# Kernel optimization log

Measured on AMD Instinct MI355X. Metric: run time of the kernel, lower is better.

## Reference

```python
import math
import jax, jax.numpy as jnp
import numpy as np

N_HEAD = 16
N_GROUPS = 32
EPS = 1e-05


def gelu(x):
    return 0.5 * x * (1.0 + jnp.tanh(math.sqrt(2.0 / math.pi) * (x + 0.044715 * x ** 3)))


def dp_group_norm(x, weight, bias, num_groups=N_GROUPS, eps=EPS):
    # x: [B, T, H]. torch F.group_norm on transposed [B, H, T] normalizes over
    # (channels_per_group, T) jointly per (batch, group).
    B, T, H = x.shape
    xg = x.reshape(B, T, num_groups, H // num_groups)
    mean = jnp.mean(xg, axis=(1, 3), keepdims=True)
    var = jnp.mean((xg - mean) ** 2, axis=(1, 3), keepdims=True)
    xn = ((xg - mean) / jnp.sqrt(var + eps)).reshape(B, T, H)
    return xn * weight + bias


def attention(x, w_attn, b_attn, w_aproj, b_aproj):
    B, T, H = x.shape
    hd = H // N_HEAD
    qkv = x @ w_attn + b_attn                      # [B, T, 3H]
    q, k, v = jnp.split(qkv, 3, axis=-1)
    q = q.reshape(B, T, N_HEAD, hd).transpose(0, 2, 1, 3)   # [B, nh, T, hd]
    k = k.reshape(B, T, N_HEAD, hd).transpose(0, 2, 1, 3)   # [B, nh, T, hd]
    v = v.reshape(B, T, N_HEAD, hd).transpose(0, 2, 1, 3)
    w = jnp.einsum('bhqd,bhkd->bhqk', q, k)        # no 1/sqrt(d): scale=False
    causal = jnp.tril(jnp.ones((T, T), dtype=x.dtype))
    w = w * causal - 1e10 * (1.0 - causal)
    w = jax.nn.softmax(w, axis=-1)
    a = jnp.einsum('bhqk,bhkd->bhqd', w, v)        # [B, nh, T, hd]
    a = a.transpose(0, 2, 1, 3).reshape(B, T, H)
    a = a @ w_aproj + b_aproj
    present = jnp.stack((k, v))                    # [2, B, nh, T, hd]
    return a, present


def setup_inputs() -> dict:
    key = jax.random.key(0)
    ks = jax.random.split(key, 6)
    B, T, H = 2, 2048, 1024
    return {
        'x': jax.random.normal(ks[0], (B, T, H), dtype=jnp.float32),
        'w_attn': jax.random.normal(ks[1], (H, 3 * H), dtype=jnp.float32) * 0.02,
        'b_attn': jnp.zeros((3 * H,), dtype=jnp.float32),
        'w_aproj': jax.random.normal(ks[2], (H, H), dtype=jnp.float32) * 0.02,
        'b_aproj': jnp.zeros((H,), dtype=jnp.float32),
        'ln1_w': jnp.ones((H,), dtype=jnp.float32),
        'ln1_b': jnp.zeros((H,), dtype=jnp.float32),
        'ln2_w': jnp.ones((H,), dtype=jnp.float32),
        'ln2_b': jnp.zeros((H,), dtype=jnp.float32),
        'w_fc': jax.random.normal(ks[3], (H, 4 * H), dtype=jnp.float32) * 0.02,
        'b_fc': jnp.zeros((4 * H,), dtype=jnp.float32),
        'w_mproj': jax.random.normal(ks[4], (4 * H, H), dtype=jnp.float32) * 0.02,
        'b_mproj': jnp.zeros((H,), dtype=jnp.float32),
    }


def reference(x, w_attn, b_attn, w_aproj, b_aproj, ln1_w, ln1_b, ln2_w, ln2_b,
              w_fc, b_fc, w_mproj, b_mproj):
    a, present = attention(dp_group_norm(x, ln1_w, ln1_b), w_attn, b_attn, w_aproj, b_aproj)
    x = x + a
    h = gelu(dp_group_norm(x, ln2_w, ln2_b) @ w_fc + b_fc)
    m = h @ w_mproj + b_mproj
    x = x + m
    return (x, present)
```

## Files before the change

kernel.cpp:

```cpp
#include <hip/hip_runtime.h>

#define B_  2
#define T_  2048
#define H_  1024
#define NH_ 16
#define HD_ 64
#define M_  (B_*T_)
#define PS_ 72

typedef __bf16 bf16x8 __attribute__((ext_vector_type(8)));
typedef float  floatx4 __attribute__((ext_vector_type(4)));

typedef __attribute__((address_space(1))) const unsigned int gas_u32;
typedef __attribute__((address_space(3))) unsigned int       las_u32;

__device__ __forceinline__ void gload_lds16(const __bf16* g, __bf16* l) {
    __builtin_amdgcn_global_load_lds((gas_u32*)g, (las_u32*)l, 16, 0, 0);
}

__global__ __launch_bounds__(256) void transpose_bf16(
    const float* __restrict__ in, __bf16* __restrict__ out, int K, int N)
{
    __shared__ float tile[32][33];
    const int k0 = blockIdx.x * 32, n0 = blockIdx.y * 32;
    const int tx = threadIdx.x & 31, ty = threadIdx.x >> 5;
#pragma unroll
    for (int i = 0; i < 32; i += 8)
        tile[ty + i][tx] = in[(size_t)(k0 + ty + i) * N + (n0 + tx)];
    __syncthreads();
#pragma unroll
    for (int i = 0; i < 32; i += 8)
        out[(size_t)(n0 + ty + i) * K + (k0 + tx)] = (__bf16)tile[tx][ty + i];
}

__global__ __launch_bounds__(256) void gn_partial(
    const float* __restrict__ x, float2* __restrict__ part)
{
    const int bg = blockIdx.x, chunk = blockIdx.y;
    const int batch = bg >> 5, g = bg & 31;
    const float* xp = x + (size_t)batch * T_ * H_ + g * 32;
    float s = 0.f, ss = 0.f;
    for (int i = threadIdx.x; i < 128 * 32; i += 256) {
        const int t = chunk * 128 + (i >> 5), c = i & 31;
        const float v = xp[(size_t)t * H_ + c];
        s += v; ss += v * v;
    }
#pragma unroll
    for (int off = 32; off > 0; off >>= 1) {
        s  += __shfl_down(s,  off, 64);
        ss += __shfl_down(ss, off, 64);
    }
    __shared__ float rs[4], rss[4];
    const int wv = threadIdx.x >> 6, lane = threadIdx.x & 63;
    if (lane == 0) { rs[wv] = s; rss[wv] = ss; }
    __syncthreads();
    if (threadIdx.x == 0)
        part[bg * 16 + chunk] =
            make_float2(rs[0] + rs[1] + rs[2] + rs[3],
                        rss[0] + rss[1] + rss[2] + rss[3]);
}

__global__ __launch_bounds__(64) void gn_finalize(
    const float2* __restrict__ part, float2* __restrict__ stats)
{
    const int bg = threadIdx.x;
    float s = 0.f, ss = 0.f;
#pragma unroll
    for (int i = 0; i < 16; ++i) {
        const float2 p = part[bg * 16 + i];
        s += p.x; ss += p.y;
    }
    const float inv = 1.f / (float)(T_ * 32);
    const float mean = s * inv;
    const float var  = ss * inv - mean * mean;
    stats[bg] = make_float2(mean, rsqrtf(var + 1e-5f));
}

__global__ __launch_bounds__(256) void gn_apply(
    const float* __restrict__ x, const float2* __restrict__ stats,
    const float* __restrict__ w, const float* __restrict__ bsc,
    __bf16* __restrict__ out)
{
    const size_t idx = ((size_t)blockIdx.x * 256 + threadIdx.x) * 4;
    const int h = (int)(idx & (H_ - 1));
    const int batch = (int)(idx >> 21);
    const float2 mr = stats[batch * 32 + (h >> 5)];
    const float4 xv = *(const float4*)(x + idx);
    const float4 wv = *(const float4*)(w + h);
    const float4 bv = *(const float4*)(bsc + h);
    __bf16 o[4];
    o[0] = (__bf16)((xv.x - mr.x) * mr.y * wv.x + bv.x);
    o[1] = (__bf16)((xv.y - mr.x) * mr.y * wv.y + bv.y);
    o[2] = (__bf16)((xv.z - mr.x) * mr.y * wv.z + bv.z);
    o[3] = (__bf16)((xv.w - mr.x) * mr.y * wv.w + bv.w);
    *(uint2*)(out + idx) = *(uint2*)o;
}

__device__ __forceinline__ void gemm_core(
    const __bf16* __restrict__ A, const __bf16* __restrict__ BT,
    int K, int m0, int n0, __bf16* As, __bf16* Bs, floatx4 (&acc)[4][4])
{
    const int tid  = threadIdx.x;
    const int lane = tid & 63, wv = tid >> 6;
    const int quad = lane >> 4, l16 = lane & 15;
    const int wm = (wv >> 1) * 64, wn = (wv & 1) * 64;
    const int r0 = tid >> 2, c0 = (tid & 3) * 8;

    const __bf16* Ag = A  + (size_t)(m0 + r0) * K + c0;
    const __bf16* Bg = BT + (size_t)(n0 + r0) * K + c0;

    for (int kt = 0; kt < K; kt += 64) {
        __syncthreads();
#pragma unroll
        for (int s = 0; s < 2; ++s) {
            gload_lds16(Ag + kt + s * 32,                As + s * 4096 + tid * 8);
            gload_lds16(Ag + (size_t)64 * K + kt + s * 32, As + s * 4096 + 2048 + tid * 8);
            gload_lds16(Bg + kt + s * 32,                Bs + s * 4096 + tid * 8);
            gload_lds16(Bg + (size_t)64 * K + kt + s * 32, Bs + s * 4096 + 2048 + tid * 8);
        }
        __syncthreads();
#pragma unroll
        for (int kk = 0; kk < 2; ++kk) {
            bf16x8 af[4], bfg[4];
#pragma unroll
            for (int i = 0; i < 4; ++i)
                af[i]  = *(const bf16x8*)(As + kk * 4096 + (wm + i * 16 + l16) * 32 + quad * 8);
#pragma unroll
            for (int i = 0; i < 4; ++i)
                bfg[i] = *(const bf16x8*)(Bs + kk * 4096 + (wn + i * 16 + l16) * 32 + quad * 8);
#pragma unroll
            for (int mi = 0; mi < 4; ++mi)
#pragma unroll
                for (int ni = 0; ni < 4; ++ni)
                    acc[mi][ni] = __builtin_amdgcn_mfma_f32_16x16x32_bf16(
                        af[mi], bfg[ni], acc[mi][ni], 0, 0, 0);
        }
    }
}

#define GEMM_PROLOGUE(KVAL)                                             \
    __shared__ __align__(16) __bf16 As[2 * 4096], Bs[2 * 4096];         \
    const int m0 = blockIdx.x * 128, n0 = blockIdx.y * 128;             \
    floatx4 acc[4][4];                                                  \
    { floatx4 z = {0.f, 0.f, 0.f, 0.f};                                 \
      for (int i = 0; i < 4; ++i) for (int j = 0; j < 4; ++j) acc[i][j] = z; } \
    gemm_core(A, BT, (KVAL), m0, n0, As, Bs, acc);                      \
    const int tid = threadIdx.x, lane = tid & 63, wv = tid >> 6;        \
    const int quad = lane >> 4, l16 = lane & 15;                        \
    const int wm = (wv >> 1) * 64, wn = (wv & 1) * 64;                  \
    (void)tid;

__global__ __launch_bounds__(256) void gemm_qkv(
    const __bf16* __restrict__ A, const __bf16* __restrict__ BT,
    const float* __restrict__ bias, __bf16* __restrict__ qb,
    __bf16* __restrict__ kb, __bf16* __restrict__ vtb,
    float* __restrict__ present)
{
    GEMM_PROLOGUE(H_)
#pragma unroll
    for (int ni = 0; ni < 4; ++ni) {
        const int col = n0 + wn + ni * 16 + l16;
        const float bv = bias[col];
        const int which = col >> 10, c = col & 1023, hh = c >> 6, d = c & 63;
#pragma unroll
        for (int mi = 0; mi < 4; ++mi)
#pragma unroll
            for (int r = 0; r < 4; ++r) {
                const int row = m0 + wm + mi * 16 + quad * 4 + r;
                const int bb = row >> 11, t = row & 2047;
                const float v = acc[mi][ni][r] + bv;
                const size_t idx = (((size_t)bb * NH_ + hh) * T_ + t) * HD_ + d;
                if (which == 0)      qb[idx] = (__bf16)(v * 1.4426950408889634f);
                else if (which == 1) { kb[idx] = (__bf16)v; present[idx] = v; }
                else { vtb[(((size_t)bb * NH_ + hh) * HD_ + d) * T_ + t] = (__bf16)v;
                       present[(size_t)B_ * NH_ * T_ * HD_ + idx] = v; }
            }
    }
}

__global__ __launch_bounds__(256) void gemm_gelu(
    const __bf16* __restrict__ A, const __bf16* __restrict__ BT,
    const float* __restrict__ bias, __bf16* __restrict__ out)
{
    GEMM_PROLOGUE(H_)
#pragma unroll
    for (int ni = 0; ni < 4; ++ni) {
        const int col = n0 + wn + ni * 16 + l16;
        const float bv = bias[col];
#pragma unroll
        for (int mi = 0; mi < 4; ++mi)
#pragma unroll
            for (int r = 0; r < 4; ++r) {
                const int row = m0 + wm + mi * 16 + quad * 4 + r;
                const float v = acc[mi][ni][r] + bv;
                const float g = 0.5f * v *
                    (1.f + tanhf(0.7978845608028654f * (v + 0.044715f * v * v * v)));
                out[(size_t)row * (4 * H_) + col] = (__bf16)g;
            }
    }
}

__global__ __launch_bounds__(256) void gemm_resid_n64(
    const __bf16* __restrict__ A, const __bf16* __restrict__ BT,
    const float* __restrict__ bias, const float* __restrict__ resid,
    float* __restrict__ out, int K, int N)
{
    __shared__ __align__(16) __bf16 As[2 * 4096], Bs[2 * 2048];
    const int m0 = blockIdx.x * 128, n0 = blockIdx.y * 64;
    const int tid  = threadIdx.x;
    const int lane = tid & 63, wv = tid >> 6;
    const int quad = lane >> 4, l16 = lane & 15;
    const int wm = (wv >> 1) * 64, wn = (wv & 1) * 32;
    const int r0 = tid >> 2, c0 = (tid & 3) * 8;

    floatx4 acc[4][2];
    { floatx4 z = {0.f, 0.f, 0.f, 0.f};
#pragma unroll
      for (int i = 0; i < 4; ++i) { acc[i][0] = z; acc[i][1] = z; } }

    const __bf16* Ag = A  + (size_t)(m0 + r0) * K + c0;
    const __bf16* Bg = BT + (size_t)(n0 + r0) * K + c0;

    for (int kt = 0; kt < K; kt += 64) {
        __syncthreads();
#pragma unroll
        for (int s = 0; s < 2; ++s) {
            gload_lds16(Ag + kt + s * 32,                  As + s * 4096 + tid * 8);
            gload_lds16(Ag + (size_t)64 * K + kt + s * 32, As + s * 4096 + 2048 + tid * 8);
            gload_lds16(Bg + kt + s * 32,                  Bs + s * 2048 + tid * 8);
        }
        __syncthreads();
#pragma unroll
        for (int kk = 0; kk < 2; ++kk) {
            bf16x8 af[4], bfg[2];
#pragma unroll
            for (int i = 0; i < 4; ++i)
                af[i]  = *(const bf16x8*)(As + kk * 4096 + (wm + i * 16 + l16) * 32 + quad * 8);
#pragma unroll
            for (int i = 0; i < 2; ++i)
                bfg[i] = *(const bf16x8*)(Bs + kk * 2048 + (wn + i * 16 + l16) * 32 + quad * 8);
#pragma unroll
            for (int mi = 0; mi < 4; ++mi)
#pragma unroll
                for (int ni = 0; ni < 2; ++ni)
                    acc[mi][ni] = __builtin_amdgcn_mfma_f32_16x16x32_bf16(
                        af[mi], bfg[ni], acc[mi][ni], 0, 0, 0);
        }
    }

#pragma unroll
    for (int ni = 0; ni < 2; ++ni) {
        const int col = n0 + wn + ni * 16 + l16;
        const float bv = bias[col];
#pragma unroll
        for (int mi = 0; mi < 4; ++mi)
#pragma unroll
            for (int r = 0; r < 4; ++r) {
                const int row = m0 + wm + mi * 16 + quad * 4 + r;
                const size_t idx = (size_t)row * N + col;
                out[idx] = acc[mi][ni][r] + bv + resid[idx];
            }
    }
}

__global__ __launch_bounds__(256) void attn_kernel(
    const __bf16* __restrict__ qb, const __bf16* __restrict__ kb,
    const __bf16* __restrict__ vtb, __bf16* __restrict__ aout)
{
    const int bh = blockIdx.x;
    const int sp = 31 - blockIdx.y;
    const int bb = bh >> 4, hh = bh & 15;
    const __bf16* Q  = qb  + (size_t)bh * T_ * HD_;
    const __bf16* Kp = kb  + (size_t)bh * T_ * HD_;
    const __bf16* VT = vtb + (size_t)bh * HD_ * T_;
    __shared__ __align__(16) __bf16 Qs[2 * 2048];
    __shared__ __align__(16) __bf16 Ks[2][2 * 2048];
    __shared__ __align__(16) __bf16 Vs[2][2 * 2048];
    __shared__ __align__(16) __bf16 Ps[64 * PS_];

    const int tid = threadIdx.x, lane = tid & 63, wv = tid >> 6;
    const int quad = lane >> 4, l16 = lane & 15;
    const int sr = tid >> 2;
    const int scs = (((tid & 3) ^ ((sr >> 1) & 3)) * 8);
    const int xq8 = (quad ^ ((l16 >> 1) & 3)) * 8;

    const int q0 = sp * 64, nkt = sp + 1;

#pragma unroll
    for (int s = 0; s < 2; ++s) {
        gload_lds16(Q  + (size_t)(q0 + sr) * HD_ + s * 32 + scs, Qs + s * 2048 + tid * 8);
        gload_lds16(Kp + (size_t)sr * HD_ + s * 32 + scs, &Ks[0][s * 2048 + tid * 8]);
        gload_lds16(VT + (size_t)sr * T_  + s * 32 + scs, &Vs[0][s * 2048 + tid * 8]);
    }
    asm volatile("s_waitcnt vmcnt(0)" ::: "memory");
    __builtin_amdgcn_s_barrier();
    __builtin_amdgcn_sched_barrier(0);

    bf16x8 aq[2];
#pragma unroll
    for (int kk = 0; kk < 2; ++kk)
        aq[kk] = *(const bf16x8*)(Qs + kk * 2048 + (wv * 16 + l16) * 32 + xq8);

    float m_i[4], l_p[4];
    floatx4 Ov[4];
    { floatx4 z = {0.f, 0.f, 0.f, 0.f};
#pragma unroll
      for (int i = 0; i < 4; ++i) { Ov[i] = z; m_i[i] = -1e30f; l_p[i] = 0.f; } }

    int cur = 0;
    for (int kt = 0; kt < nkt; ++kt) {
        if (kt + 1 < nkt) {
            const int kn = (kt + 1) * 64;
#pragma unroll
            for (int s = 0; s < 2; ++s) {
                gload_lds16(Kp + (size_t)(kn + sr) * HD_ + s * 32 + scs,
                            &Ks[cur ^ 1][s * 2048 + tid * 8]);
                gload_lds16(VT + (size_t)sr * T_ + kn + s * 32 + scs,
                            &Vs[cur ^ 1][s * 2048 + tid * 8]);
            }
            asm volatile("s_waitcnt vmcnt(4)" ::: "memory");
        } else {
            asm volatile("s_waitcnt vmcnt(0)" ::: "memory");
        }
        __builtin_amdgcn_s_barrier();
        __builtin_amdgcn_sched_barrier(0);

        const __bf16* Kc = Ks[cur];
        const __bf16* Vc = Vs[cur];

        floatx4 sacc[4];
        { floatx4 z = {0.f, 0.f, 0.f, 0.f};
#pragma unroll
          for (int i = 0; i < 4; ++i) sacc[i] = z; }
#pragma unroll
        for (int kk = 0; kk < 2; ++kk)
#pragma unroll
            for (int ni = 0; ni < 4; ++ni) {
                const bf16x8 bk = *(const bf16x8*)(Kc + kk * 2048 + (ni * 16 + l16) * 32 + xq8);
                sacc[ni] = __builtin_amdgcn_mfma_f32_16x16x32_bf16(aq[kk], bk, sacc[ni], 0, 0, 0);
            }
        if (kt == sp) {
#pragma unroll
            for (int ni = 0; ni < 4; ++ni) {
                const int keyL = ni * 16 + l16;
#pragma unroll
                for (int r = 0; r < 4; ++r)
                    if (keyL > quad * 4 + r + wv * 16) sacc[ni][r] = -1e30f;
            }
        }
        float rmax[4];
#pragma unroll
        for (int r = 0; r < 4; ++r)
            rmax[r] = fmaxf(fmaxf(sacc[0][r], sacc[1][r]),
                            fmaxf(sacc[2][r], sacc[3][r]));
#pragma unroll
        for (int off = 1; off < 16; off <<= 1)
#pragma unroll
            for (int r = 0; r < 4; ++r)
                rmax[r] = fmaxf(rmax[r], __shfl_xor(rmax[r], off, 64));
        float need = rmax[0] - m_i[0];
#pragma unroll
        for (int r = 1; r < 4; ++r) need = fmaxf(need, rmax[r] - m_i[r]);
        if (__any(need > 8.f)) {
#pragma unroll
            for (int r = 0; r < 4; ++r) {
                const float mn = fmaxf(m_i[r], rmax[r]);
                const float al = exp2f(m_i[r] - mn);
                m_i[r] = mn;
                l_p[r] *= al;
#pragma unroll
                for (int ni = 0; ni < 4; ++ni) Ov[ni][r] *= al;
            }
        }
#pragma unroll
        for (int ni = 0; ni < 4; ++ni)
#pragma unroll
            for (int r = 0; r < 4; ++r) {
                const float pe = exp2f(sacc[ni][r] - m_i[r]);
                sacc[ni][r] = pe;
                l_p[r] += pe;
            }
#pragma unroll
        for (int ni = 0; ni < 4; ++ni)
#pragma unroll
            for (int r = 0; r < 4; ++r)
                Ps[(wv * 16 + quad * 4 + r) * PS_ + ni * 16 + l16] = (__bf16)sacc[ni][r];
#pragma unroll
        for (int kk = 0; kk < 2; ++kk) {
            const bf16x8 ap = *(const bf16x8*)(Ps + (wv * 16 + l16) * PS_ + kk * 32 + quad * 8);
#pragma unroll
            for (int ni = 0; ni < 4; ++ni) {
                const bf16x8 bv2 = *(const bf16x8*)(Vc + kk * 2048 + (ni * 16 + l16) * 32 + xq8);
                Ov[ni] = __builtin_amdgcn_mfma_f32_16x16x32_bf16(ap, bv2, Ov[ni], 0, 0, 0);
            }
        }
        __builtin_amdgcn_sched_barrier(0);
        __builtin_amdgcn_s_barrier();
        __builtin_amdgcn_sched_barrier(0);
        cur ^= 1;
    }
#pragma unroll
    for (int off = 1; off < 16; off <<= 1)
#pragma unroll
        for (int r = 0; r < 4; ++r)
            l_p[r] += __shfl_xor(l_p[r], off, 64);
#pragma unroll
    for (int ni = 0; ni < 4; ++ni)
#pragma unroll
        for (int r = 0; r < 4; ++r) {
            const int t = q0 + wv * 16 + quad * 4 + r;
            aout[((size_t)(bb * T_ + t)) * H_ + hh * HD_ + ni * 16 + l16] =
                (__bf16)(Ov[ni][r] / l_p[r]);
        }
}

extern "C" void kernel_launch(void* const* d_in, const int* in_sizes, int n_in,
                              void* d_out, int out_size, void* d_ws, size_t ws_size,
                              hipStream_t stream)
{
    (void)in_sizes; (void)n_in; (void)out_size; (void)ws_size;
    const float* x       = (const float*)d_in[0];
    const float* w_attn  = (const float*)d_in[1];
    const float* b_attn  = (const float*)d_in[2];
    const float* w_aproj = (const float*)d_in[3];
    const float* b_aproj = (const float*)d_in[4];
    const float* ln1_w   = (const float*)d_in[5];
    const float* ln1_b   = (const float*)d_in[6];
    const float* ln2_w   = (const float*)d_in[7];
    const float* ln2_b   = (const float*)d_in[8];
    const float* w_fc    = (const float*)d_in[9];
    const float* b_fc    = (const float*)d_in[10];
    const float* w_mproj = (const float*)d_in[11];
    const float* b_mproj = (const float*)d_in[12];
    float* out = (float*)d_out;
    float* present = out + (size_t)M_ * H_;

    char* wp = (char*)d_ws;
    auto alloc = [&](size_t bytes) {
        void* p = (void*)wp; wp += (bytes + 255) & ~(size_t)255; return p;
    };
    __bf16* A1       = (__bf16*)alloc((size_t)M_ * H_ * 2);
    __bf16* A2       = (__bf16*)alloc((size_t)M_ * H_ * 2);
    __bf16* WattnT   = (__bf16*)alloc((size_t)3 * H_ * H_ * 2);
    __bf16* WaprojT  = (__bf16*)alloc((size_t)H_ * H_ * 2);
    __bf16* WfcT     = (__bf16*)alloc((size_t)4 * H_ * H_ * 2);
    __bf16* WmprojT  = (__bf16*)alloc((size_t)4 * H_ * H_ * 2);
    __bf16* qb       = (__bf16*)alloc((size_t)M_ * H_ * 2);
    __bf16* kb       = (__bf16*)alloc((size_t)M_ * H_ * 2);
    __bf16* vtb      = (__bf16*)alloc((size_t)M_ * H_ * 2);
    __bf16* attn_out = (__bf16*)alloc((size_t)M_ * H_ * 2);
    float*  x2       = (float*) alloc((size_t)M_ * H_ * 4);
    __bf16* Hbuf     = (__bf16*)alloc((size_t)M_ * 4 * H_ * 2);
    float2* gn_part  = (float2*)alloc(64 * 16 * sizeof(float2));
    float2* gn_stats = (float2*)alloc(64 * sizeof(float2));

    transpose_bf16<<<dim3(H_/32, 3*H_/32), 256, 0, stream>>>(w_attn,  WattnT,  H_,   3*H_);
    transpose_bf16<<<dim3(H_/32, H_/32),   256, 0, stream>>>(w_aproj, WaprojT, H_,   H_);
    transpose_bf16<<<dim3(H_/32, 4*H_/32), 256, 0, stream>>>(w_fc,    WfcT,    H_,   4*H_);
    transpose_bf16<<<dim3(4*H_/32, H_/32), 256, 0, stream>>>(w_mproj, WmprojT, 4*H_, H_);

    gn_partial <<<dim3(64, 16), 256, 0, stream>>>(x, gn_part);
    gn_finalize<<<1, 64, 0, stream>>>(gn_part, gn_stats);
    gn_apply   <<<M_*H_/1024, 256, 0, stream>>>(x, gn_stats, ln1_w, ln1_b, A1);

    gemm_qkv<<<dim3(M_/128, 3*H_/128), 256, 0, stream>>>(A1, WattnT, b_attn,
                                                         qb, kb, vtb, present);
    attn_kernel<<<dim3(32, 32), 256, 0, stream>>>(qb, kb, vtb, attn_out);
    gemm_resid_n64<<<dim3(M_/128, H_/64), 256, 0, stream>>>(attn_out, WaprojT, b_aproj,
                                                            x, x2, H_, H_);

    gn_partial <<<dim3(64, 16), 256, 0, stream>>>(x2, gn_part);
    gn_finalize<<<1, 64, 0, stream>>>(gn_part, gn_stats);
    gn_apply   <<<M_*H_/1024, 256, 0, stream>>>(x2, gn_stats, ln2_w, ln2_b, A2);

    gemm_gelu<<<dim3(M_/128, 4*H_/128), 256, 0, stream>>>(A2, WfcT, b_fc, Hbuf);
    gemm_resid_n64<<<dim3(M_/128, H_/64), 256, 0, stream>>>(Hbuf, WmprojT, b_mproj,
                                                            x2, out, 4*H_, H_);
}
```

Baseline: 419.9 us.

## Double-buffer GEMM LDS tiles with XOR swizzle and cheaper GELU

The GEMM mainloops (shared core and the N=64 residual GEMM) now double-buffer their LDS tiles. The next K-tile is prefetched with global_load_lds while MFMAs run on the current one, synchronised with explicit vmcnt waits and raw barriers. Tile columns are XOR-swizzled on the global side so that each lane's 16-byte chunk lands at a swizzled LDS slot, with matching reads, to reduce LDS bank conflicts. GELU's tanh is rewritten as x*sigmoid(2u) using exp2 and a hardware reciprocal. Together these double LDS usage, which may lower occupancy, and rely on hand-counted vmcnt values being right.

```diff
diff --git a/kernel.cpp b/kernel.cpp
--- a/kernel.cpp
+++ b/kernel.cpp
@@ -104,30 +104,49 @@
     const int lane = tid & 63, wv = tid >> 6;
     const int quad = lane >> 4, l16 = lane & 15;
     const int wm = (wv >> 1) * 64, wn = (wv & 1) * 64;
-    const int r0 = tid >> 2, c0 = (tid & 3) * 8;
-
-    const __bf16* Ag = A  + (size_t)(m0 + r0) * K + c0;
-    const __bf16* Bg = BT + (size_t)(n0 + r0) * K + c0;
-
+    const int r0 = tid >> 2;
+    const int scs = (((tid & 3) ^ ((r0 >> 1) & 3)) * 8);
+    const int xq8 = (quad ^ ((l16 >> 1) & 3)) * 8;
+
+    const __bf16* Ag = A  + (size_t)(m0 + r0) * K + scs;
+    const __bf16* Bg = BT + (size_t)(n0 + r0) * K + scs;
+
+#pragma unroll
+    for (int s = 0; s < 2; ++s) {
+        gload_lds16(Ag + s * 32,                  As + s * 4096 + tid * 8);
+        gload_lds16(Ag + (size_t)64 * K + s * 32, As + s * 4096 + 2048 + tid * 8);
+        gload_lds16(Bg + s * 32,                  Bs + s * 4096 + tid * 8);
+        gload_lds16(Bg + (size_t)64 * K + s * 32, Bs + s * 4096 + 2048 + tid * 8);
+    }
+    int cur = 0;
     for (int kt = 0; kt < K; kt += 64) {
-        __syncthreads();
-#pragma unroll
-        for (int s = 0; s < 2; ++s) {
-            gload_lds16(Ag + kt + s * 32,                As + s * 4096 + tid * 8);
-            gload_lds16(Ag + (size_t)64 * K + kt + s * 32, As + s * 4096 + 2048 + tid * 8);
-            gload_lds16(Bg + kt + s * 32,                Bs + s * 4096 + tid * 8);
-            gload_lds16(Bg + (size_t)64 * K + kt + s * 32, Bs + s * 4096 + 2048 + tid * 8);
-        }
-        __syncthreads();
+        if (kt + 64 < K) {
+            const int nb = (cur ^ 1) * 8192;
+            const int kn = kt + 64;
+#pragma unroll
+            for (int s = 0; s < 2; ++s) {
+                gload_lds16(Ag + kn + s * 32,                  As + nb + s * 4096 + tid * 8);
+                gload_lds16(Ag + (size_t)64 * K + kn + s * 32, As + nb + s * 4096 + 2048 + tid * 8);
+                gload_lds16(Bg + kn + s * 32,                  Bs + nb + s * 4096 + tid * 8);
+                gload_lds16(Bg + (size_t)64 * K + kn + s * 32, Bs + nb + s * 4096 + 2048 + tid * 8);
+            }
+            asm volatile("s_waitcnt vmcnt(8)" ::: "memory");
+        } else {
+            asm volatile("s_waitcnt vmcnt(0)" ::: "memory");
+        }
+        __builtin_amdgcn_s_barrier();
+        __builtin_amdgcn_sched_barrier(0);
+        const __bf16* Ab = As + cur * 8192;
+        const __bf16* Bb = Bs + cur * 8192;
 #pragma unroll
         for (int kk = 0; kk < 2; ++kk) {
             bf16x8 af[4], bfg[4];
 #pragma unroll
             for (int i = 0; i < 4; ++i)
-                af[i]  = *(const bf16x8*)(As + kk * 4096 + (wm + i * 16 + l16) * 32 + quad * 8);
+                af[i]  = *(const bf16x8*)(Ab + kk * 4096 + (wm + i * 16 + l16) * 32 + xq8);
 #pragma unroll
             for (int i = 0; i < 4; ++i)
-                bfg[i] = *(const bf16x8*)(Bs + kk * 4096 + (wn + i * 16 + l16) * 32 + quad * 8);
+                bfg[i] = *(const bf16x8*)(Bb + kk * 4096 + (wn + i * 16 + l16) * 32 + xq8);
 #pragma unroll
             for (int mi = 0; mi < 4; ++mi)
 #pragma unroll
@@ -135,11 +154,15 @@
                     acc[mi][ni] = __builtin_amdgcn_mfma_f32_16x16x32_bf16(
                         af[mi], bfg[ni], acc[mi][ni], 0, 0, 0);
         }
+        __builtin_amdgcn_sched_barrier(0);
+        __builtin_amdgcn_s_barrier();
+        __builtin_amdgcn_sched_barrier(0);
+        cur ^= 1;
     }
 }
 
 #define GEMM_PROLOGUE(KVAL)                                             \
-    __shared__ __align__(16) __bf16 As[2 * 4096], Bs[2 * 4096];         \
+    __shared__ __align__(16) __bf16 As[2 * 8192], Bs[2 * 8192];         \
     const int m0 = blockIdx.x * 128, n0 = blockIdx.y * 128;             \
     floatx4 acc[4][4];                                                  \
     { floatx4 z = {0.f, 0.f, 0.f, 0.f};                                 \
@@ -193,9 +216,10 @@
             for (int r = 0; r < 4; ++r) {
                 const int row = m0 + wm + mi * 16 + quad * 4 + r;
                 const float v = acc[mi][ni][r] + bv;
-                const float g = 0.5f * v *
-                    (1.f + tanhf(0.7978845608028654f * (v + 0.044715f * v * v * v)));
-                out[(size_t)row * (4 * H_) + col] = (__bf16)g;
+                const float e = exp2f(-2.3022082f * (v + 0.044715f * v * v * v));
+                float rcp;
+                asm("v_rcp_f32 %0, %1" : "=v"(rcp) : "v"(1.f + e));
+                out[(size_t)row * (4 * H_) + col] = (__bf16)(v * rcp);
             }
     }
 }
@@ -205,40 +229,58 @@
     const float* __restrict__ bias, const float* __restrict__ resid,
     float* __restrict__ out, int K, int N)
 {
-    __shared__ __align__(16) __bf16 As[2 * 4096], Bs[2 * 2048];
+    __shared__ __align__(16) __bf16 As[2 * 8192], Bs[2 * 4096];
     const int m0 = blockIdx.x * 128, n0 = blockIdx.y * 64;
     const int tid  = threadIdx.x;
     const int lane = tid & 63, wv = tid >> 6;
     const int quad = lane >> 4, l16 = lane & 15;
     const int wm = (wv >> 1) * 64, wn = (wv & 1) * 32;
-    const int r0 = tid >> 2, c0 = (tid & 3) * 8;
+    const int r0 = tid >> 2;
+    const int scs = (((tid & 3) ^ ((r0 >> 1) & 3)) * 8);
+    const int xq8 = (quad ^ ((l16 >> 1) & 3)) * 8;
 
     floatx4 acc[4][2];
     { floatx4 z = {0.f, 0.f, 0.f, 0.f};
 #pragma unroll
       for (int i = 0; i < 4; ++i) { acc[i][0] = z; acc[i][1] = z; } }
 
-    const __bf16* Ag = A  + (size_t)(m0 + r0) * K + c0;
-    const __bf16* Bg = BT + (size_t)(n0 + r0) * K + c0;
-
+    const __bf16* Ag = A  + (size_t)(m0 + r0) * K + scs;
+    const __bf16* Bg = BT + (size_t)(n0 + r0) * K + scs;
+
+#pragma unroll
+    for (int s = 0; s < 2; ++s) {
+        gload_lds16(Ag + s * 32,                  As + s * 4096 + tid * 8);
+        gload_lds16(Ag + (size_t)64 * K + s * 32, As + s * 4096 + 2048 + tid * 8);
+        gload_lds16(Bg + s * 32,                  Bs + s * 2048 + tid * 8);
+    }
+    int cur = 0;
     for (int kt = 0; kt < K; kt += 64) {
-        __syncthreads();
-#pragma unroll
-        for (int s = 0; s < 2; ++s) {
-            gload_lds16(Ag + kt + s * 32,                  As + s * 4096 + tid * 8);
-            gload_lds16(Ag + (size_t)64 * K + kt + s * 32, As + s * 4096 + 2048 + tid * 8);
-            gload_lds16(Bg + kt + s * 32,                  Bs + s * 2048 + tid * 8);
-        }
-        __syncthreads();
+        if (kt + 64 < K) {
+            const int kn = kt + 64;
+            const int nbA = (cur ^ 1) * 8192, nbB = (cur ^ 1) * 4096;
+#pragma unroll
+            for (int s = 0; s < 2; ++s) {
+                gload_lds16(Ag + kn + s * 32,                  As + nbA + s * 4096 + tid * 8);
+                gload_lds16(Ag + (size_t)64 * K + kn + s * 32, As + nbA + s * 4096 + 2048 + tid * 8);
+                gload_lds16(Bg + kn + s * 32,                  Bs + nbB + s * 2048 + tid * 8);
+            }
+            asm volatile("s_waitcnt vmcnt(6)" ::: "memory");
+        } else {
+            asm volatile("s_waitcnt vmcnt(0)" ::: "memory");
+        }
+        __builtin_amdgcn_s_barrier();
+        __builtin_amdgcn_sched_barrier(0);
+        const __bf16* Ab = As + cur * 8192;
+        const __bf16* Bb = Bs + cur * 4096;
 #pragma unroll
         for (int kk = 0; kk < 2; ++kk) {
             bf16x8 af[4], bfg[2];
 #pragma unroll
             for (int i = 0; i < 4; ++i)
-                af[i]  = *(const bf16x8*)(As + kk * 4096 + (wm + i * 16 + l16) * 32 + quad * 8);
+                af[i]  = *(const bf16x8*)(Ab + kk * 4096 + (wm + i * 16 + l16) * 32 + xq8);
 #pragma unroll
             for (int i = 0; i < 2; ++i)
-                bfg[i] = *(const bf16x8*)(Bs + kk * 2048 + (wn + i * 16 + l16) * 32 + quad * 8);
+                bfg[i] = *(const bf16x8*)(Bb + kk * 2048 + (wn + i * 16 + l16) * 32 + xq8);
 #pragma unroll
             for (int mi = 0; mi < 4; ++mi)
 #pragma unroll
@@ -246,6 +288,10 @@
                     acc[mi][ni] = __builtin_amdgcn_mfma_f32_16x16x32_bf16(
                         af[mi], bfg[ni], acc[mi][ni], 0, 0, 0);
         }
+        __builtin_amdgcn_sched_barrier(0);
+        __builtin_amdgcn_s_barrier();
+        __builtin_amdgcn_sched_barrier(0);
+        cur ^= 1;
     }
 
 #pragma unroll
```

Result: faster. 409.9 us (-2.4%).
